# Kernel optimization log

Hardware: AMD Instinct MI355X
Metric: run time of the kernel (lower is better)

The kernel has to match this reference:

```python
import jax, jax.numpy as jnp
import numpy as np

# CSV_Architecture_v2 layout (per frame, 130 floats):
#   hand 0 block: [0]=handedness label, [1]=handedness prob, [2:65]=21*3 coords
#   hand 1 block: [65]=handedness label, [66]=handedness prob, [67:130]=coords
POS0, PROB0 = 0, 1
POS1, PROB1 = 65, 66
HAND_LEN = 65
FRAME_LEN = 2 * HAND_LEN


def _build_swap_pattern():
    all_idxs = np.arange(FRAME_LEN)
    idxs_0 = np.arange(0, HAND_LEN)
    idxs_1 = np.arange(HAND_LEN, FRAME_LEN)
    all_idxs[idxs_0], all_idxs[idxs_1] = all_idxs[idxs_1].copy(), all_idxs[idxs_0].copy()
    return jnp.asarray(all_idxs, dtype=jnp.int32)


def setup_inputs() -> dict:
    key = jax.random.key(0)
    B, S = 256, 1024
    X = jax.random.normal(key, (B, S, FRAME_LEN), dtype=jnp.float32)
    return {"X": X, "swap_pattern": _build_swap_pattern()}


def reference(X, swap_pattern):
    # Per-frame handedness labels / probabilities.
    h0 = X[..., POS0]
    h1 = X[..., POS1]
    p0 = X[..., PROB0]
    p1 = X[..., PROB1]

    nan0 = jnp.isnan(h0)
    nan1 = jnp.isnan(h1)
    no_nan = jnp.logical_and(~nan0, ~nan1)

    one = jnp.float32(1.0)
    zero = jnp.float32(0.0)

    # skip1: hands already ordered (right label > left label)
    skip1 = h1 > h0
    # skip2: both predictions NaN -> no hands detected
    skip2 = jnp.logical_and(nan0, nan1)
    # skip3: only hand 1 present, labeled right (==1)
    skip3 = jnp.logical_and(nan0, h1 == one)
    # skip4: only hand 0 present, labeled left (==0)
    skip4 = jnp.logical_and(nan1, h0 == zero)
    eq = h0 == h1
    # skip5: both labeled left, position-0 hand has higher prob
    skip5 = no_nan & eq & (h0 == zero) & (p0 > p1)
    # skip6: both labeled right, position-1 hand has higher prob
    skip6 = no_nan & eq & (h0 == one) & (p0 < p1)

    skip = skip1 | skip2 | skip3 | skip4 | skip5 | skip6

    # Vectorized replacement of nested tf.map_fn: gather-permute the frame
    # representation where a swap is required.
    swapped = X[..., swap_pattern]  # [B, S, FRAME_LEN]
    return jnp.where(skip[..., None], X, swapped)
```

## Files before the change

### kernel.cpp

```cpp
#include <hip/hip_runtime.h>

constexpr int FRAME_LEN = 130;
constexpr int HALF      = 65;
constexpr int BLOCK     = 256;
constexpr int FPB       = 32;
constexpr int CHUNK_F   = FPB * FRAME_LEN;
constexpr int CHUNK_F2  = CHUNK_F / 2;

__device__ __forceinline__ int div130(int idx) {
    return (int)(((unsigned)idx * 8067u) >> 20);
}

__device__ __forceinline__ bool skip_pred(float h0, float p0, float h1, float p1) {
    const bool nan0 = (h0 != h0);
    const bool nan1 = (h1 != h1);
    const bool no_nan = !nan0 && !nan1;
    const bool eq = (h0 == h1);
    return (h1 > h0) ||
           (nan0 && nan1) ||
           (nan0 && (h1 == 1.0f)) ||
           (nan1 && (h0 == 0.0f)) ||
           (no_nan && eq && (h0 == 0.0f) && (p0 > p1)) ||
           (no_nan && eq && (h0 == 1.0f) && (p0 < p1));
}

__device__ __forceinline__ float2 make_out2(const float* __restrict__ Xb,
                                            unsigned mask, int g) {
    const int idx = 2 * g;
    const int fl  = div130(idx);
    const int jj  = idx - fl * FRAME_LEN;
    const bool sk = (mask >> fl) & 1u;
    const int d0  = sk ? 0 : (jj     < HALF ?  HALF : -HALF);
    const int d1  = sk ? 0 : (jj + 1 < HALF ?  HALF : -HALF);
    const int fbase = fl * FRAME_LEN;
    float2 r;
    r.x = Xb[fbase + jj     + d0];
    r.y = Xb[fbase + jj + 1 + d1];
    return r;
}

__global__ __launch_bounds__(BLOCK, 8)
void hand_sorter_kernel(const float* __restrict__ X, float* __restrict__ out,
                        int n_frames) {
    const int t = threadIdx.x;
    const long long frame0 = (long long)blockIdx.x * FPB;
    const long long rem = (long long)n_frames - frame0;
    const int frames_here = rem < (long long)FPB ? (int)rem : FPB;
    const long long base = frame0 * (long long)FRAME_LEN;
    const float* __restrict__ Xb = X + base;
    float* __restrict__ Ob = out + base;

    if (frames_here == FPB) {
        const int lane = t & 63;
        bool pred = false;
        if (lane < FPB) {
            const float* fr = Xb + lane * FRAME_LEN;
            const float2 a = *(const float2*)fr;
            const float2 b = *(const float2*)(fr + 64);
            const float2 c = *(const float2*)(fr + 66);
            pred = skip_pred(a.x, a.y, b.y, c.x);
        }
        const unsigned mask = (unsigned)__ballot(pred);

        float2* __restrict__ Ov = (float2*)Ob;

#pragma unroll
        for (int k = 0; k < 8; ++k) {
            const int g = t + k * 256;
            Ov[g] = make_out2(Xb, mask, g);
        }
        {
            const int g = t + 2048;
            if (g < CHUNK_F2) Ov[g] = make_out2(Xb, mask, g);
        }
    } else {
        const int nf = frames_here * FRAME_LEN;
        for (int i = t; i < nf; i += BLOCK) {
            const int fle = div130(i);
            const int je  = i - fle * FRAME_LEN;
            const float* fr = Xb + fle * FRAME_LEN;
            const bool sk = skip_pred(fr[0], fr[1], fr[HALF], fr[HALF + 1]);
            int sj = je + (sk ? 0 : (je < HALF ? HALF : -HALF));
            Ob[i] = fr[sj];
        }
    }
}

extern "C" void kernel_launch(void* const* d_in, const int* in_sizes, int n_in,
                              void* d_out, int out_size, void* d_ws, size_t ws_size,
                              hipStream_t stream) {
    const float* X = (const float*)d_in[0];
    float* out = (float*)d_out;
    const int n_frames = in_sizes[0] / FRAME_LEN;
    const int n_blocks = (n_frames + FPB - 1) / FPB;
    hand_sorter_kernel<<<n_blocks, BLOCK, 0, stream>>>(X, out, n_frames);
}
```

Before: 245.1 us.

## Vectorize hand-swap gather to 16-byte loads with register shuffles

Replaces the per-float2 scalar gathers with 16-byte vector loads. Each thread loads two adjacent aligned float4 vectors at the swapped source offset and assembles its output with register shuffles, falling back to scalar gathers only for vectors that straddle frame or hand boundaries. All loads are issued before any stores and pinned in registers with an empty asm barrier to raise memory-level parallelism. Launch bounds are relaxed to allow more registers, which may lower occupancy.

```diff
diff --git a/kernel.cpp b/kernel.cpp
--- a/kernel.cpp
+++ b/kernel.cpp
@@ -5,7 +5,9 @@
 constexpr int BLOCK     = 256;
 constexpr int FPB       = 32;
 constexpr int CHUNK_F   = FPB * FRAME_LEN;
-constexpr int CHUNK_F2  = CHUNK_F / 2;
+constexpr int CHUNK_V4  = CHUNK_F / 4;
+
+typedef float v4f __attribute__((ext_vector_type(4)));
 
 __device__ __forceinline__ int div130(int idx) {
     return (int)(((unsigned)idx * 8067u) >> 20);
@@ -24,22 +26,7 @@
            (no_nan && eq && (h0 == 1.0f) && (p0 < p1));
 }
 
-__device__ __forceinline__ float2 make_out2(const float* __restrict__ Xb,
-                                            unsigned mask, int g) {
-    const int idx = 2 * g;
-    const int fl  = div130(idx);
-    const int jj  = idx - fl * FRAME_LEN;
-    const bool sk = (mask >> fl) & 1u;
-    const int d0  = sk ? 0 : (jj     < HALF ?  HALF : -HALF);
-    const int d1  = sk ? 0 : (jj + 1 < HALF ?  HALF : -HALF);
-    const int fbase = fl * FRAME_LEN;
-    float2 r;
-    r.x = Xb[fbase + jj     + d0];
-    r.y = Xb[fbase + jj + 1 + d1];
-    return r;
-}
-
-__global__ __launch_bounds__(BLOCK, 8)
+__global__ __launch_bounds__(BLOCK, 4)
 void hand_sorter_kernel(const float* __restrict__ X, float* __restrict__ out,
                         int n_frames) {
     const int t = threadIdx.x;
@@ -55,24 +42,80 @@
         bool pred = false;
         if (lane < FPB) {
             const float* fr = Xb + lane * FRAME_LEN;
-            const float2 a = *(const float2*)fr;
-            const float2 b = *(const float2*)(fr + 64);
-            const float2 c = *(const float2*)(fr + 66);
-            pred = skip_pred(a.x, a.y, b.y, c.x);
+            const v4f a = *(const v4f*)fr;
+            const v4f b = *(const v4f*)(fr + 64);
+            pred = skip_pred(a.x, a.y, b.y, b.z);
         }
         const unsigned mask = (unsigned)__ballot(pred);
 
-        float2* __restrict__ Ov = (float2*)Ob;
+        const v4f* __restrict__ Xv = (const v4f*)Xb;
+        v4f* __restrict__ Ov = (v4f*)Ob;
 
-#pragma unroll
-        for (int k = 0; k < 8; ++k) {
-            const int g = t + k * 256;
-            Ov[g] = make_out2(Xb, mask, g);
+        v4f va0, va1, va2, va3, va4, vb0, vb1, vb2, vb3, vb4;
+#define LOAD_PAIR(K, VA, VB)                                              \
+        {                                                                 \
+            const int i0 = t + (K) * 256;                                 \
+            const int i  = ((K) < 4 || i0 < CHUNK_V4) ? i0 : 0;           \
+            const int idx = 4 * i;                                        \
+            const int fl  = div130(idx);                                  \
+            const int jj  = idx - fl * FRAME_LEN;                         \
+            const bool skipf = (mask >> fl) & 1u;                         \
+            const bool lo = (jj < HALF);                                  \
+            int s = idx + (skipf ? 0 : (lo ? HALF : -HALF));              \
+            int a = s >> 2;                                               \
+            if (a > CHUNK_V4 - 1) a = CHUNK_V4 - 1;                       \
+            int a1 = a + 1;                                               \
+            if (a1 > CHUNK_V4 - 1) a1 = CHUNK_V4 - 1;                     \
+            VA = Xv[a];                                                   \
+            VB = Xv[a1];                                                  \
         }
-        {
-            const int g = t + 2048;
-            if (g < CHUNK_F2) Ov[g] = make_out2(Xb, mask, g);
+        LOAD_PAIR(0, va0, vb0)
+        LOAD_PAIR(1, va1, vb1)
+        LOAD_PAIR(2, va2, vb2)
+        LOAD_PAIR(3, va3, vb3)
+        LOAD_PAIR(4, va4, vb4)
+#undef LOAD_PAIR
+
+        asm volatile("" : "+v"(va0), "+v"(va1), "+v"(va2), "+v"(va3), "+v"(va4),
+                          "+v"(vb0), "+v"(vb1), "+v"(vb2), "+v"(vb3), "+v"(vb4));
+
+#define EMIT(K, VA, VB)                                                   \
+        {                                                                 \
+            const int i = t + (K) * 256;                                  \
+            if ((K) < 4 || i < CHUNK_V4) {                                \
+                const int idx = 4 * i;                                    \
+                const int fl  = div130(idx);                              \
+                const int jj  = idx - fl * FRAME_LEN;                     \
+                const bool fast = (jj <= FRAME_LEN - 4) &&                \
+                                  (jj < HALF - 3 || jj >= HALF);          \
+                v4f r;                                                    \
+                if (fast) {                                               \
+                    const bool skipf = (mask >> fl) & 1u;                 \
+                    const bool lo = (jj < HALF);                          \
+                    v4f f1; f1.x = VA.y; f1.y = VA.z; f1.z = VA.w; f1.w = VB.x; \
+                    v4f f3; f3.x = VA.w; f3.y = VB.x; f3.z = VB.y; f3.w = VB.z; \
+                    const v4f swp = lo ? f1 : f3;                         \
+                    r = skipf ? VA : swp;                                 \
+                } else {                                                  \
+                    _Pragma("unroll")                                     \
+                    for (int e = 0; e < 4; ++e) {                         \
+                        const int ide = idx + e;                          \
+                        const int fle = div130(ide);                      \
+                        const int je  = ide - fle * FRAME_LEN;            \
+                        const bool sk = (mask >> fle) & 1u;               \
+                        const int sj = je + (sk ? 0 : (je < HALF ? HALF : -HALF)); \
+                        ((float*)&r)[e] = Xb[fle * FRAME_LEN + sj];       \
+                    }                                                     \
+                }                                                         \
+                Ov[i] = r;                                                \
+            }                                                             \
         }
+        EMIT(0, va0, vb0)
+        EMIT(1, va1, vb1)
+        EMIT(2, va2, vb2)
+        EMIT(3, va3, vb3)
+        EMIT(4, va4, vb4)
+#undef EMIT
     } else {
         const int nf = frames_here * FRAME_LEN;
         for (int i = t; i < nf; i += BLOCK) {
```

New measurement: 241.5 us. Within noise of the previous version (-1.5%).

## Use persistent grid with software-pipelined chunk loads and header prefetch

Applied to the files above, without the earlier changes.

Replaces one-block-per-32-frames with a persistent grid capped at 1024 blocks that strides over chunks. Each step prefetches the header of the chunk two ahead, loads the next chunk into registers while storing the current one, and uses an empty asm barrier to keep the loaded values in registers. The aim is to overlap load latency with stores and cut launch and block-scheduling overhead in this memory-bound permute. In exchange it raises register use, lowers occupancy to 4 blocks per SIMD, and moves the tail frames to block 0.

```diff
diff --git a/kernel.cpp b/kernel.cpp
--- a/kernel.cpp
+++ b/kernel.cpp
@@ -6,6 +6,9 @@
 constexpr int FPB       = 32;
 constexpr int CHUNK_F   = FPB * FRAME_LEN;
 constexpr int CHUNK_F2  = CHUNK_F / 2;
+constexpr int MAXGRID   = 1024;
+
+typedef float v4f __attribute__((ext_vector_type(4), aligned(4)));
 
 __device__ __forceinline__ int div130(int idx) {
     return (int)(((unsigned)idx * 8067u) >> 20);
@@ -24,64 +27,106 @@
            (no_nan && eq && (h0 == 1.0f) && (p0 < p1));
 }
 
-__device__ __forceinline__ float2 make_out2(const float* __restrict__ Xb,
-                                            unsigned mask, int g) {
-    const int idx = 2 * g;
-    const int fl  = div130(idx);
-    const int jj  = idx - fl * FRAME_LEN;
-    const bool sk = (mask >> fl) & 1u;
-    const int d0  = sk ? 0 : (jj     < HALF ?  HALF : -HALF);
-    const int d1  = sk ? 0 : (jj + 1 < HALF ?  HALF : -HALF);
-    const int fbase = fl * FRAME_LEN;
-    float2 r;
-    r.x = Xb[fbase + jj     + d0];
-    r.y = Xb[fbase + jj + 1 + d1];
-    return r;
+__device__ __forceinline__ void issue_hdr(const float* __restrict__ X, long long cid,
+                                          int lane, v4f& ha, v4f& hb) {
+    const float* fr = X + cid * CHUNK_F + (lane & 31) * FRAME_LEN;
+    ha = *(const v4f*)fr;
+    hb = *(const v4f*)(fr + 64);
 }
 
-__global__ __launch_bounds__(BLOCK, 8)
+__device__ __forceinline__ void load_chunk(const float* __restrict__ Xb,
+                                           unsigned mask, int t, float2 (&r)[9]) {
+#pragma unroll
+    for (int k = 0; k < 9; ++k) {
+        const int g = (k < 8) ? (t + k * 256) : ((t & 31) + 2048);
+        const int idx = 2 * g;
+        const int fl  = div130(idx);
+        const int jj  = idx - fl * FRAME_LEN;
+        const bool sk = (mask >> fl) & 1u;
+        const int d0  = sk ? 0 : (jj     < HALF ? HALF : -HALF);
+        const int d1  = sk ? 0 : (jj + 1 < HALF ? HALF : -HALF);
+        const int fb  = fl * FRAME_LEN;
+        r[k].x = Xb[fb + jj     + d0];
+        r[k].y = Xb[fb + jj + 1 + d1];
+    }
+}
+
+__device__ __forceinline__ void pin9(float2 (&r)[9]) {
+    asm volatile("" : "+v"(r[0]), "+v"(r[1]), "+v"(r[2]), "+v"(r[3]), "+v"(r[4]),
+                      "+v"(r[5]), "+v"(r[6]), "+v"(r[7]), "+v"(r[8]));
+}
+
+__device__ __forceinline__ void store_chunk(float* __restrict__ Ob, int t,
+                                            float2 (&r)[9]) {
+    float2* __restrict__ Ov = (float2*)Ob;
+#pragma unroll
+    for (int k = 0; k < 8; ++k) Ov[t + k * 256] = r[k];
+    if (t < CHUNK_F2 - 2048) Ov[t + 2048] = r[8];
+}
+
+template <int CUR, int NXT>
+__device__ __forceinline__ bool pipe_step(const float* __restrict__ X,
+        float* __restrict__ out, long long& c, long long G, long long full,
+        int t, int lane, float2 (&r)[2][9], unsigned (&msk)[2], v4f (&hd)[2][2]) {
+    const long long cn = c + G;
+    const bool more = (cn < full);
+    if (more) {
+        const long long cnn = cn + G;
+        if (cnn < full)
+            issue_hdr(X, cnn, lane, hd[CUR][0], hd[CUR][1]);
+        msk[NXT] = (unsigned)__ballot(
+            skip_pred(hd[NXT][0].x, hd[NXT][0].y, hd[NXT][1].y, hd[NXT][1].z));
+        load_chunk(X + cn * CHUNK_F, msk[NXT], t, r[NXT]);
+        pin9(r[NXT]);
+    }
+    store_chunk(out + c * CHUNK_F, t, r[CUR]);
+    c = cn;
+    return !more;
+}
+
+__global__ __launch_bounds__(BLOCK, 4)
 void hand_sorter_kernel(const float* __restrict__ X, float* __restrict__ out,
                         int n_frames) {
     const int t = threadIdx.x;
-    const long long frame0 = (long long)blockIdx.x * FPB;
-    const long long rem = (long long)n_frames - frame0;
-    const int frames_here = rem < (long long)FPB ? (int)rem : FPB;
-    const long long base = frame0 * (long long)FRAME_LEN;
-    const float* __restrict__ Xb = X + base;
-    float* __restrict__ Ob = out + base;
+    const int lane = t & 63;
+    const long long full = n_frames / FPB;
+    const long long G = gridDim.x;
+    long long c = blockIdx.x;
 
-    if (frames_here == FPB) {
-        const int lane = t & 63;
-        bool pred = false;
-        if (lane < FPB) {
-            const float* fr = Xb + lane * FRAME_LEN;
-            const float2 a = *(const float2*)fr;
-            const float2 b = *(const float2*)(fr + 64);
-            const float2 c = *(const float2*)(fr + 66);
-            pred = skip_pred(a.x, a.y, b.y, c.x);
+    if (c < full) {
+        float2 r[2][9];
+        unsigned msk[2];
+        v4f hd[2][2];
+
+        issue_hdr(X, c, lane, hd[0][0], hd[0][1]);
+        msk[0] = (unsigned)__ballot(
+            skip_pred(hd[0][0].x, hd[0][0].y, hd[0][1].y, hd[0][1].z));
+        if (c + G < full)
+            issue_hdr(X, c + G, lane, hd[1][0], hd[1][1]);
+        load_chunk(X + c * CHUNK_F, msk[0], t, r[0]);
+        pin9(r[0]);
+
+        while (true) {
+            if (pipe_step<0, 1>(X, out, c, G, full, t, lane, r, msk, hd)) break;
+            if (pipe_step<1, 0>(X, out, c, G, full, t, lane, r, msk, hd)) break;
         }
-        const unsigned mask = (unsigned)__ballot(pred);
+    }
 
-        float2* __restrict__ Ov = (float2*)Ob;
-
-#pragma unroll
-        for (int k = 0; k < 8; ++k) {
-            const int g = t + k * 256;
-            Ov[g] = make_out2(Xb, mask, g);
-        }
-        {
-            const int g = t + 2048;
-            if (g < CHUNK_F2) Ov[g] = make_out2(Xb, mask, g);
-        }
-    } else {
-        const int nf = frames_here * FRAME_LEN;
-        for (int i = t; i < nf; i += BLOCK) {
-            const int fle = div130(i);
-            const int je  = i - fle * FRAME_LEN;
-            const float* fr = Xb + fle * FRAME_LEN;
-            const bool sk = skip_pred(fr[0], fr[1], fr[HALF], fr[HALF + 1]);
-            int sj = je + (sk ? 0 : (je < HALF ? HALF : -HALF));
-            Ob[i] = fr[sj];
+    if (blockIdx.x == 0) {
+        const int nrem = n_frames - (int)(full * FPB);
+        if (nrem > 0) {
+            const long long base = full * (long long)CHUNK_F;
+            const float* __restrict__ Xb = X + base;
+            float* __restrict__ Ob = out + base;
+            const int nf = nrem * FRAME_LEN;
+            for (int i = t; i < nf; i += BLOCK) {
+                const int fle = div130(i);
+                const int je  = i - fle * FRAME_LEN;
+                const float* fr = Xb + fle * FRAME_LEN;
+                const bool sk = skip_pred(fr[0], fr[1], fr[HALF], fr[HALF + 1]);
+                const int sj = je + (sk ? 0 : (je < HALF ? HALF : -HALF));
+                Ob[i] = fr[sj];
+            }
         }
     }
 }
@@ -92,6 +137,7 @@
     const float* X = (const float*)d_in[0];
     float* out = (float*)d_out;
     const int n_frames = in_sizes[0] / FRAME_LEN;
-    const int n_blocks = (n_frames + FPB - 1) / FPB;
+    const long long full = n_frames / FPB;
+    int n_blocks = (int)(full < MAXGRID ? (full > 0 ? full : 1) : MAXGRID);
     hand_sorter_kernel<<<n_blocks, BLOCK, 0, stream>>>(X, out, n_frames);
 }
```

Result: no change. 247.9 us (+1.1%).
